# Optimization experiments

Measured on AMD Instinct MI355X. Metric: run time of the kernel, lower is better.

The kernel has to match this reference:

```python
import jax, jax.numpy as jnp
from jax import lax
import numpy as np

B, C, H, W = 16, 128, 128, 128
S1 = C // 2   # 64, LKA3 branch channels
S2 = C - S1   # 64, LKA5 branch channels
EPS = 1e-6
DN = ('NCHW', 'OIHW', 'NCHW')


def _dw(x, w, b, pad, dil=1):
    # depthwise conv; torch weight layout (C,1,kh,kw) == OIHW with groups=C
    y = lax.conv_general_dilated(x, w, (1, 1), [(pad[0], pad[0]), (pad[1], pad[1])],
                                 rhs_dilation=(dil, dil), dimension_numbers=DN,
                                 feature_group_count=w.shape[0])
    return y + b[None, :, None, None]


def _pw(x, w, b):
    # 1x1 pointwise conv
    y = lax.conv_general_dilated(x, w, (1, 1), [(0, 0), (0, 0)], dimension_numbers=DN)
    return y + b[None, :, None, None]


def setup_inputs() -> dict:
    key = jax.random.key(0)
    ks = iter(jax.random.split(key, 40))
    rn = lambda shape, s=0.05: jax.random.normal(next(ks), shape, jnp.float32) * s
    inp = {
        'x': jax.random.normal(next(ks), (B, C, H, W), jnp.float32),
        'ln_w': jnp.ones((C,), jnp.float32),
        'ln_b': jnp.zeros((C,), jnp.float32),
        'scale': rn((1, C, 1, 1)),
        'pf_w': rn((2 * C, C, 1, 1)), 'pf_b': rn((2 * C,)),
        # LKA3: dw(1x3) -> dw(3x1) -> dw5 dil2 -> 1x1
        'lka3_w1': rn((S1, 1, 1, 3)), 'lka3_b1': rn((S1,)),
        'lka3_w2': rn((S1, 1, 3, 1)), 'lka3_b2': rn((S1,)),
        'lka3_w3': rn((S1, 1, 5, 5)), 'lka3_b3': rn((S1,)),
        'lka3_w4': rn((S1, S1, 1, 1)), 'lka3_b4': rn((S1,)),
        # LKA5: dw5 -> dw7 dil2 -> 1x1
        'lka5_w1': rn((S2, 1, 5, 5)), 'lka5_b1': rn((S2,)),
        'lka5_w2': rn((S2, 1, 7, 7)), 'lka5_b2': rn((S2,)),
        'lka5_w3': rn((S2, S2, 1, 1)), 'lka5_b3': rn((S2,)),
        # gating convs
        'x3a_w': rn((S1, 1, 1, 3)), 'x3a_b': rn((S1,)),
        'x3b_w': rn((S1, 1, 3, 1)), 'x3b_b': rn((S1,)),
        'x5_w': rn((S2, 1, 5, 5)), 'x5_b': rn((S2,)),
        'pl_w': rn((C, C, 1, 1)), 'pl_b': rn((C,)),
    }
    return inp


def reference(x, ln_w, ln_b, scale, pf_w, pf_b,
              lka3_w1, lka3_b1, lka3_w2, lka3_b2, lka3_w3, lka3_b3, lka3_w4, lka3_b4,
              lka5_w1, lka5_b1, lka5_w2, lka5_b2, lka5_w3, lka5_b3,
              x3a_w, x3a_b, x3b_w, x3b_b, x5_w, x5_b, pl_w, pl_b):
    shortcut = x
    # channels_first LayerNorm (biased variance over channel dim)
    u = jnp.mean(x, axis=1, keepdims=True)
    s = jnp.mean((x - u) ** 2, axis=1, keepdims=True)
    xn = (x - u) * lax.rsqrt(s + EPS)
    xn = ln_w[None, :, None, None] * xn + ln_b[None, :, None, None]
    # proj_first: C -> 2C
    h = _pw(xn, pf_w, pf_b)
    a, xh = h[:, :C], h[:, C:]
    a1, a2 = a[:, :S1], a[:, S1:]
    # gating branch for a1: 1x3 then 3x1 depthwise
    x3_out = _dw(_dw(a1, x3a_w, x3a_b, (0, 1)), x3b_w, x3b_b, (1, 0))
    # LKA3: dw(1x3)->dw(3x1)->dw5(dil2,pad4)->1x1
    l3 = _dw(a1, lka3_w1, lka3_b1, (0, 1))
    l3 = _dw(l3, lka3_w2, lka3_b2, (1, 0))
    l3 = _dw(l3, lka3_w3, lka3_b3, (4, 4), dil=2)
    l3 = _pw(l3, lka3_w4, lka3_b4)
    attn_1 = l3 * x3_out
    # LKA5: dw5(pad2)->dw7(dil2,pad6)->1x1
    l5 = _dw(a2, lka5_w1, lka5_b1, (2, 2))
    l5 = _dw(l5, lka5_w2, lka5_b2, (6, 6), dil=2)
    l5 = _pw(l5, lka5_w3, lka5_b3)
    attn_2 = l5 * _dw(a2, x5_w, x5_b, (2, 2))
    a = jnp.concatenate([attn_1, attn_2], axis=1)
    out = _pw(xh * a, pl_w, pl_b) * scale + shortcut
    return out
```

## Files before the change

### kernel.cpp

```cpp
#include <hip/hip_runtime.h>
#include <hip/hip_bf16.h>

typedef __hip_bfloat16 bf16;
typedef unsigned short ushort_t;
typedef float f32x4 __attribute__((ext_vector_type(4)));
typedef short bf16x8 __attribute__((ext_vector_type(8)));
typedef ushort_t u16x4 __attribute__((ext_vector_type(4)));

#define MFMA16(a, b, c) __builtin_amdgcn_mfma_f32_16x16x32_bf16(a, b, c, 0, 0, 0)

__device__ inline ushort_t f2b(float f) {
  bf16 h = __float2bfloat16(f);
  return __builtin_bit_cast(ushort_t, h);
}
__device__ inline float b2f(ushort_t u) {
  bf16 h = __builtin_bit_cast(bf16, u);
  return __bfloat162float(h);
}
__device__ inline float blo(unsigned d) { return __builtin_bit_cast(float, d << 16); }
__device__ inline float bhi(unsigned d) { return __builtin_bit_cast(float, d & 0xffff0000u); }


__global__ __launch_bounds__(256) void prepack_pf(
    const float* __restrict__ pf_w, ushort_t* __restrict__ pf_wp)
{
  int idx = blockIdx.x * 256 + threadIdx.x;
  int j = idx & 7, lane = (idx >> 3) & 63, kc = (idx >> 9) & 3, t = idx >> 11;
  int oc = t * 16 + (lane & 15), ic = kc * 32 + (lane >> 4) * 8 + j;
  pf_wp[idx] = f2b(pf_w[oc * 128 + ic]);
}

__global__ __launch_bounds__(256) void prepack_small(
    const float* __restrict__ w4, const float* __restrict__ w5,
    const float* __restrict__ plw, ushort_t* __restrict__ dst)
{
  int idx = blockIdx.x * 256 + threadIdx.x;
  if (idx < 8192) {
    const float* src = (idx < 4096) ? w4 : w5;
    int k = idx & 4095;
    int j = k & 7, lane = (k >> 3) & 63, kc = (k >> 9) & 1, t = k >> 10;
    int oc = t * 16 + (lane & 15), ic = kc * 32 + (lane >> 4) * 8 + j;
    dst[idx] = f2b(src[oc * 64 + ic]);
  } else {
    int k = idx - 8192;
    int j = k & 7, lane = (k >> 3) & 63, kc = (k >> 9) & 3, t = k >> 11;
    int oc = t * 16 + (lane & 15), ic = kc * 32 + (lane >> 4) * 8 + j;
    dst[idx] = f2b(plw[oc * 128 + ic]);
  }
}

__global__ __launch_bounds__(256) void ln_pf_mfma(
    const float* __restrict__ x, const float* __restrict__ ln_w,
    const float* __restrict__ ln_b, const ushort_t* __restrict__ pf_wp,
    const float* __restrict__ pf_b, ushort_t* __restrict__ h)
{
  __shared__ __attribute__((aligned(16))) unsigned char sm[34816];
  ushort_t* xs = (ushort_t*)sm;
  float* red = (float*)(sm + 17408);
  float* mrs = (float*)(sm + 17408 + 2048);

  const int tid = threadIdx.x;
  const int p = tid & 63, cg = tid >> 6;
  const int g0 = blockIdx.x * 64;
  const int b = g0 >> 14, hw0 = g0 & 16383;
  const float* xp = x + (long)b * (128L * 16384) + hw0 + p;

  float v[32];
  #pragma unroll
  for (int i = 0; i < 32; ++i) v[i] = xp[(long)(cg * 32 + i) * 16384];
  float s = 0.f, ss = 0.f;
  #pragma unroll
  for (int i = 0; i < 32; ++i) { s += v[i]; ss += v[i] * v[i]; }
  red[cg * 64 + p] = s;
  red[256 + cg * 64 + p] = ss;
  __syncthreads();
  if (tid < 64) {
    float st = red[tid] + red[64 + tid] + red[128 + tid] + red[192 + tid];
    float sst = red[256 + tid] + red[320 + tid] + red[384 + tid] + red[448 + tid];
    float m = st * 0.0078125f;
    float var = sst * 0.0078125f - m * m;
    mrs[tid] = m;
    mrs[64 + tid] = rsqrtf(var + 1e-6f);
  }
  __syncthreads();
  {
    float m = mrs[p], rs = mrs[64 + p];
    #pragma unroll
    for (int i = 0; i < 32; ++i) {
      int c = cg * 32 + i;
      xs[p * 136 + c] = f2b((v[i] - m) * rs * ln_w[c] + ln_b[c]);
    }
  }
  __syncthreads();

  const int l = tid & 63, lm = l & 15, q = l >> 4;
  const int wv = __builtin_amdgcn_readfirstlane(tid >> 6);
  f32x4 acc[4][4];
  #pragma unroll
  for (int a = 0; a < 4; ++a)
    #pragma unroll
    for (int n = 0; n < 4; ++n) acc[a][n] = {0.f, 0.f, 0.f, 0.f};

  #pragma unroll
  for (int kc = 0; kc < 4; ++kc) {
    bf16x8 af[4], bfr[4];
    #pragma unroll
    for (int mt = 0; mt < 4; ++mt)
      af[mt] = *(const bf16x8*)&xs[(mt * 16 + lm) * 136 + kc * 32 + q * 8];
    #pragma unroll
    for (int nt = 0; nt < 4; ++nt)
      bfr[nt] = *(const bf16x8*)&pf_wp[(((wv * 4 + nt) * 4 + kc) * 64 + l) * 8];
    #pragma unroll
    for (int mt = 0; mt < 4; ++mt)
      #pragma unroll
      for (int nt = 0; nt < 4; ++nt)
        acc[mt][nt] = MFMA16(af[mt], bfr[nt], acc[mt][nt]);
  }
  __syncthreads();

  ushort_t* hst = (ushort_t*)sm;
  #pragma unroll
  for (int nt = 0; nt < 4; ++nt) {
    int oc = wv * 64 + nt * 16 + lm;
    float bias = pf_b[oc];
    #pragma unroll
    for (int mt = 0; mt < 4; ++mt) {
      int px0 = mt * 16 + q * 4;
      union { ushort_t u[4]; uint2 w; } pk;
      #pragma unroll
      for (int r = 0; r < 4; ++r) pk.u[r] = f2b(acc[mt][nt][r] + bias);
      *(uint2*)&hst[oc * 68 + px0] = pk.w;
    }
  }
  __syncthreads();
  {
    int px = (tid & 31) * 2;
    int ocb = tid >> 5;
    ushort_t* hp = h + (long)b * 256 * 16384 + hw0 + px;
    #pragma unroll
    for (int i = 0; i < 32; ++i) {
      int oc = ocb + 8 * i;
      *(unsigned*)(hp + (long)oc * 16384) = *(unsigned*)&hst[oc * 68 + px];
    }
  }
}

__global__ __launch_bounds__(256) void dw_branch1_kernel(
    const bf16* __restrict__ hbuf,
    const float* __restrict__ w1, const float* __restrict__ b1,
    const float* __restrict__ w2, const float* __restrict__ b2,
    const float* __restrict__ w3, const float* __restrict__ b3,
    const float* __restrict__ wa, const float* __restrict__ ba,
    const float* __restrict__ wb, const float* __restrict__ bb,
    bf16* __restrict__ d3, bf16* __restrict__ x3o)
{
  __shared__ __attribute__((aligned(16))) unsigned char smem[28000];
  float* st1 = (float*)smem;
  float* st2 = (float*)(smem + 14560);
  ushort_t* sa = (ushort_t*)(smem + 14560);
  unsigned* sad = (unsigned*)sa;

  const int t = blockIdx.x;
  const int band = t & 7, c = (t >> 3) & 63, b = t >> 9;
  const int y0 = band * 16;
  const int tid = threadIdx.x;
  const bf16* ap = hbuf + ((long)b * 256 + c) * 16384;

  for (int i = tid; i < 26 * 16; i += 256) {
    int r = i >> 4, j = i & 15;
    int dw = (j < 4) ? j : (64 + j);
    sad[r * 80 + dw] = 0u;
  }
  {
    const int lane = tid & 63, w = tid >> 6;
    #pragma unroll
    for (int i = 0; i < 7; ++i) {
      int rr = w + 4 * i;
      if (rr < 26) {
        int gy = y0 - 5 + rr;
        unsigned val = 0u;
        if ((unsigned)gy < 128u) val = *(const unsigned*)(ap + gy * 128 + lane * 2);
        sad[rr * 80 + 4 + lane] = val;
      }
    }
  }
  __syncthreads();

  {
    float W0 = w1[c * 3], Wm = w1[c * 3 + 1], Wp = w1[c * 3 + 2];
    const float B1v = b1[c];
    for (int task = tid; task < 26 * 17; task += 256) {
      int r = task / 17, g = task - r * 17;
      int c0 = g * 8;
      const unsigned* sr = sad + r * 80 + (c0 >> 1) + 1;
      unsigned e0 = sr[0], e1 = sr[1], e2 = sr[2], e3 = sr[3], e4 = sr[4], e5 = sr[5];
      float vw[12];
      vw[0] = blo(e0); vw[1] = bhi(e0); vw[2] = blo(e1); vw[3] = bhi(e1);
      vw[4] = blo(e2); vw[5] = bhi(e2); vw[6] = blo(e3); vw[7] = bhi(e3);
      vw[8] = blo(e4); vw[9] = bhi(e4); vw[10] = blo(e5); vw[11] = bhi(e5);
      int gy = y0 - 5 + r;
      bool rok = (unsigned)gy < 128u;
      float* dst = &st1[r * 140 + c0];
      #pragma unroll
      for (int j = 0; j < 8; ++j) {
        float v = W0 * vw[j + 1] + Wm * vw[j + 2] + Wp * vw[j + 3] + B1v;
        int xx = c0 - 4 + j;
        dst[j] = (rok && (unsigned)xx < 128u) ? v : 0.f;
      }
    }
  }

  const int tx = tid & 15, ty = tid >> 4;
  const int x0 = tx * 8;
  const int y = y0 + ty;

  {
    float A0 = wa[c * 3], A1 = wa[c * 3 + 1], A2 = wa[c * 3 + 2];
    float Bv0 = wb[c * 3], Bv1 = wb[c * 3 + 1], Bv2 = wb[c * 3 + 2];
    const float BAv = ba[c], BBv = bb[c];
    float su[3][8];
    #pragma unroll
    for (int dy = 0; dy < 3; ++dy) {
      int gy2 = y - 1 + dy;
      int srow = ty + 4 + dy;
      const unsigned* sr = sad + srow * 80 + (x0 >> 1) + 3;
      unsigned e0 = sr[0], e1 = sr[1], e2 = sr[2], e3 = sr[3], e4 = sr[4], e5 = sr[5];
      float vw[12];
      vw[0] = blo(e0); vw[1] = bhi(e0); vw[2] = blo(e1); vw[3] = bhi(e1);
      vw[4] = blo(e2); vw[5] = bhi(e2); vw[6] = blo(e3); vw[7] = bhi(e3);
      vw[8] = blo(e4); vw[9] = bhi(e4); vw[10] = blo(e5); vw[11] = bhi(e5);
      bool rok = (unsigned)gy2 < 128u;
      #pragma unroll
      for (int j = 0; j < 8; ++j) {
        float v = A0 * vw[j + 1] + A1 * vw[j + 2] + A2 * vw[j + 3] + BAv;
        su[dy][j] = rok ? v : 0.f;
      }
    }
    union { ushort_t u[8]; uint4 v; } pk;
    #pragma unroll
    for (int j = 0; j < 8; ++j)
      pk.u[j] = f2b(Bv0 * su[0][j] + Bv1 * su[1][j] + Bv2 * su[2][j] + BBv);
    bf16* x3p = x3o + ((long)b * 64 + c) * 16384;
    *(uint4*)(x3p + y * 128 + x0) = pk.v;
  }
  __syncthreads();

  {
    float W0 = w2[c * 3], Wm = w2[c * 3 + 1], Wp = w2[c * 3 + 2];
    const float B2v = b2[c];
    for (int task = tid; task < 24 * 17; task += 256) {
      int q = task / 17, g = task - q * 17;
      int c0 = g * 8;
      const float* r0 = &st1[q * 140 + c0];
      const float* r1 = &st1[(q + 1) * 140 + c0];
      const float* r2 = &st1[(q + 2) * 140 + c0];
      int gy = y0 - 4 + q;
      bool rok = (unsigned)gy < 128u;
      float* dst = &st2[q * 140 + c0];
      #pragma unroll
      for (int j = 0; j < 8; ++j) {
        float v = W0 * r0[j] + Wm * r1[j] + Wp * r2[j] + B2v;
        int xx = c0 - 4 + j;
        dst[j] = (rok && (unsigned)xx < 128u) ? v : 0.f;
      }
    }
  }
  __syncthreads();

  {
    float W[25];
    #pragma unroll
    for (int k = 0; k < 25; ++k) W[k] = w3[c * 25 + k];
    float acc[8];
    #pragma unroll
    for (int j = 0; j < 8; ++j) acc[j] = b3[c];
    #pragma unroll
    for (int u = 0; u < 5; ++u) {
      const float* svr = &st2[(ty + 2 * u) * 140 + x0];
      float vw[16];
      #pragma unroll
      for (int k = 0; k < 16; ++k) vw[k] = svr[k];
      #pragma unroll
      for (int vv = 0; vv < 5; ++vv)
        #pragma unroll
        for (int j = 0; j < 8; ++j)
          acc[j] += W[u * 5 + vv] * vw[j + 2 * vv];
    }
    union { ushort_t u[8]; uint4 v; } pk;
    #pragma unroll
    for (int j = 0; j < 8; ++j) pk.u[j] = f2b(acc[j]);
    bf16* d3p = d3 + ((long)b * 64 + c) * 16384;
    *(uint4*)(d3p + y * 128 + x0) = pk.v;
  }
}

__global__ __launch_bounds__(256) void dw_branch2_kernel(
    const bf16* __restrict__ hbuf,
    const float* __restrict__ w1, const float* __restrict__ b1,
    const float* __restrict__ w2, const float* __restrict__ b2,
    const float* __restrict__ w5, const float* __restrict__ b5,
    bf16* __restrict__ d5, bf16* __restrict__ x5o)
{
  __shared__ ushort_t sa[32 * 160];
  __shared__ float sv[28 * 148];

  const int t = blockIdx.x;
  const int band = t & 7, c = (t >> 3) & 63, b = t >> 9;
  const int y0 = band * 16;
  const int tid = threadIdx.x;
  const bf16* ap = hbuf + ((long)b * 256 + 64 + c) * 16384;

  unsigned* sad = (unsigned*)sa;
  for (int i = tid; i < 32 * 16; i += 256) {
    int r = i >> 4, j = i & 15;
    int dw = (j < 4) ? j : (64 + j);
    sad[r * 80 + dw] = 0u;
  }
  {
    const int lane = tid & 63, w = tid >> 6;
    #pragma unroll
    for (int i = 0; i < 8; ++i) {
      int rr = w + 4 * i;
      int gy = y0 - 8 + rr;
      unsigned val = 0u;
      if ((unsigned)gy < 128u) val = *(const unsigned*)(ap + gy * 128 + lane * 2);
      sad[rr * 80 + 4 + lane] = val;
    }
  }
  __syncthreads();

  {
    float W[25];
    #pragma unroll
    for (int k = 0; k < 25; ++k) W[k] = w1[c * 25 + k];
    const float B1v = b1[c];
    for (int task = tid; task < 28 * 18; task += 256) {
      int r = task / 18, g = task - r * 18;
      int c0 = g * 8;
      float acc[8];
      #pragma unroll
      for (int j = 0; j < 8; ++j) acc[j] = B1v;
      #pragma unroll
      for (int u = 0; u < 5; ++u) {
        const unsigned* sr = sad + (r + u) * 80 + (c0 >> 1);
        unsigned e0 = sr[0], e1 = sr[1], e2 = sr[2], e3 = sr[3], e4 = sr[4], e5 = sr[5];
        float vw[12];
        vw[0] = blo(e0); vw[1] = bhi(e0); vw[2] = blo(e1); vw[3] = bhi(e1);
        vw[4] = blo(e2); vw[5] = bhi(e2); vw[6] = blo(e3); vw[7] = bhi(e3);
        vw[8] = blo(e4); vw[9] = bhi(e4); vw[10] = blo(e5); vw[11] = bhi(e5);
        #pragma unroll
        for (int v5 = 0; v5 < 5; ++v5)
          #pragma unroll
          for (int j = 0; j < 8; ++j)
            acc[j] += W[u * 5 + v5] * vw[j + v5];
      }
      int gy = y0 - 6 + r;
      bool rok = (unsigned)gy < 128u;
      float* svr = &sv[r * 148 + c0];
      #pragma unroll
      for (int j = 0; j < 8; ++j) {
        int xx = c0 + j - 6;
        svr[j] = (rok && (unsigned)xx < 128u) ? acc[j] : 0.f;
      }
    }
  }

  const int tx = tid & 15, ty = tid >> 4;
  const int x0 = tx * 8;
  const int y = y0 + ty;

  {
    float W[25];
    #pragma unroll
    for (int k = 0; k < 25; ++k) W[k] = w5[c * 25 + k];
    float acc[8];
    #pragma unroll
    for (int j = 0; j < 8; ++j) acc[j] = b5[c];
    #pragma unroll
    for (int u = 0; u < 5; ++u) {
      const unsigned* sr = sad + (ty + 6 + u) * 80 + (x0 >> 1);
      unsigned e0 = sr[3], e1 = sr[4], e2 = sr[5], e3 = sr[6], e4 = sr[7], e5 = sr[8];
      float vw[12];
      vw[0] = blo(e0); vw[1] = bhi(e0); vw[2] = blo(e1); vw[3] = bhi(e1);
      vw[4] = blo(e2); vw[5] = bhi(e2); vw[6] = blo(e3); vw[7] = bhi(e3);
      vw[8] = blo(e4); vw[9] = bhi(e4); vw[10] = blo(e5); vw[11] = bhi(e5);
      #pragma unroll
      for (int v5 = 0; v5 < 5; ++v5)
        #pragma unroll
        for (int j = 0; j < 8; ++j)
          acc[j] += W[u * 5 + v5] * vw[j + v5];
    }
    union { ushort_t u[8]; uint4 v; } pk;
    #pragma unroll
    for (int j = 0; j < 8; ++j) pk.u[j] = f2b(acc[j]);
    bf16* x5p = x5o + ((long)b * 64 + c) * 16384;
    *(uint4*)(x5p + y * 128 + x0) = pk.v;
  }
  __syncthreads();

  {
    float W[49];
    #pragma unroll
    for (int k = 0; k < 49; ++k) W[k] = w2[c * 49 + k];
    float acc[8];
    #pragma unroll
    for (int j = 0; j < 8; ++j) acc[j] = b2[c];
    #pragma unroll
    for (int u = 0; u < 7; ++u) {
      const float* svr = &sv[(ty + 2 * u) * 148 + x0];
      float vw[20];
      #pragma unroll
      for (int k = 0; k < 20; ++k) vw[k] = svr[k];
      #pragma unroll
      for (int vv = 0; vv < 7; ++vv)
        #pragma unroll
        for (int j = 0; j < 8; ++j)
          acc[j] += W[u * 7 + vv] * vw[j + 2 * vv];
    }
    union { ushort_t u[8]; uint4 v; } pk;
    #pragma unroll
    for (int j = 0; j < 8; ++j) pk.u[j] = f2b(acc[j]);
    bf16* d5p = d5 + ((long)b * 64 + c) * 16384;
    *(uint4*)(d5p + y * 128 + x0) = pk.v;
  }
}

__global__ __launch_bounds__(256) void final_mfma(
    const ushort_t* __restrict__ h, const ushort_t* __restrict__ d3,
    const ushort_t* __restrict__ x3o, const ushort_t* __restrict__ d5,
    const ushort_t* __restrict__ x5o,
    const ushort_t* __restrict__ w4p, const float* __restrict__ b4,
    const ushort_t* __restrict__ w5p, const float* __restrict__ b5,
    const ushort_t* __restrict__ plwp, const float* __restrict__ plb,
    const float* __restrict__ scale, const float* __restrict__ x,
    float* __restrict__ out)
{
  __shared__ __attribute__((aligned(16))) unsigned char sm[53248];
  ushort_t* A3 = (ushort_t*)sm;
  ushort_t* A5 = (ushort_t*)(sm + 9216);
  ushort_t* gA = (ushort_t*)sm;
  ushort_t* X3 = (ushort_t*)(sm + 18432);
  ushort_t* X5 = (ushort_t*)(sm + 27136);
  ushort_t* XH = (ushort_t*)(sm + 35840);
  float* outL  = (float*)(sm + 18432);

  const int tid = threadIdx.x;
  const int g0 = blockIdx.x * 64;
  const int b = g0 >> 14, hw0 = g0 & 16383;
  const long base64 = (long)b * 64 * 16384 + hw0;
  const long base256 = (long)b * 256 * 16384 + hw0;
  const int p = tid & 63;
  const int p2 = (tid & 31) * 2, cg8 = tid >> 5;

  unsigned xhreg[16];
  #pragma unroll
  for (int i = 0; i < 16; ++i) {
    int ch = cg8 + 8 * i;
    xhreg[i] = *(const unsigned*)&h[base256 + (long)(128 + ch) * 16384 + p2];
  }

  #pragma unroll
  for (int i = 0; i < 8; ++i) {
    int ch = (tid >> 6) * 2 + 8 * i;
    unsigned v3 = (unsigned)d3[base64 + (long)ch * 16384 + p] |
                  ((unsigned)d3[base64 + (long)(ch + 1) * 16384 + p] << 16);
    unsigned v5 = (unsigned)d5[base64 + (long)ch * 16384 + p] |
                  ((unsigned)d5[base64 + (long)(ch + 1) * 16384 + p] << 16);
    *(unsigned*)&A3[p * 72 + ch] = v3;
    *(unsigned*)&A5[p * 72 + ch] = v5;
  }
  #pragma unroll
  for (int i = 0; i < 8; ++i) {
    int ch = cg8 + 8 * i;
    *(unsigned*)&X3[ch * 68 + p2] = *(const unsigned*)&x3o[base64 + (long)ch * 16384 + p2];
    *(unsigned*)&X5[ch * 68 + p2] = *(const unsigned*)&x5o[base64 + (long)ch * 16384 + p2];
  }
  __syncthreads();

  const int l = tid & 63, lm = l & 15, q = l >> 4;
  const int wv = __builtin_amdgcn_readfirstlane(tid >> 6);

  f32x4 ac1[4], ac2[4];
  #pragma unroll
  for (int n = 0; n < 4; ++n) { ac1[n] = {0.f,0.f,0.f,0.f}; ac2[n] = {0.f,0.f,0.f,0.f}; }
  #pragma unroll
  for (int kc = 0; kc < 2; ++kc) {
    bf16x8 a3f = *(const bf16x8*)&A3[(wv * 16 + lm) * 72 + kc * 32 + q * 8];
    bf16x8 a5f = *(const bf16x8*)&A5[(wv * 16 + lm) * 72 + kc * 32 + q * 8];
    #pragma unroll
    for (int nt = 0; nt < 4; ++nt) {
      bf16x8 bw4 = *(const bf16x8*)&w4p[((nt * 2 + kc) * 64 + l) * 8];
      bf16x8 bw5 = *(const bf16x8*)&w5p[((nt * 2 + kc) * 64 + l) * 8];
      ac1[nt] = MFMA16(a3f, bw4, ac1[nt]);
      ac2[nt] = MFMA16(a5f, bw5, ac2[nt]);
    }
  }

  #pragma unroll
  for (int i = 0; i < 16; ++i) {
    int ch = cg8 + 8 * i;
    *(unsigned*)&XH[ch * 68 + p2] = xhreg[i];
  }
  __syncthreads();

  {
    const int pxb = wv * 16 + q * 4;
    #pragma unroll
    for (int nt = 0; nt < 4; ++nt) {
      int oc = nt * 16 + lm;
      float bb1 = b4[oc], bb2 = b5[oc];
      u16x4 x3v = *(const u16x4*)&X3[oc * 68 + pxb];
      u16x4 x5v = *(const u16x4*)&X5[oc * 68 + pxb];
      u16x4 h1v = *(const u16x4*)&XH[oc * 68 + pxb];
      u16x4 h2v = *(const u16x4*)&XH[(64 + oc) * 68 + pxb];
      #pragma unroll
      for (int r = 0; r < 4; ++r) {
        float at1 = (ac1[nt][r] + bb1) * b2f(x3v[r]);
        float at2 = (ac2[nt][r] + bb2) * b2f(x5v[r]);
        float g1 = b2f(h1v[r]) * at1;
        float g2 = b2f(h2v[r]) * at2;
        gA[(pxb + r) * 136 + oc]      = f2b(g1);
        gA[(pxb + r) * 136 + 64 + oc] = f2b(g2);
      }
    }
  }
  __syncthreads();

  f32x4 ap[4][2];
  #pragma unroll
  for (int mt = 0; mt < 4; ++mt) { ap[mt][0] = {0.f,0.f,0.f,0.f}; ap[mt][1] = {0.f,0.f,0.f,0.f}; }
  #pragma unroll
  for (int kc = 0; kc < 4; ++kc) {
    bf16x8 af[4];
    #pragma unroll
    for (int mt = 0; mt < 4; ++mt)
      af[mt] = *(const bf16x8*)&gA[(mt * 16 + lm) * 136 + kc * 32 + q * 8];
    #pragma unroll
    for (int j = 0; j < 2; ++j) {
      bf16x8 bp = *(const bf16x8*)&plwp[(((wv * 2 + j) * 4 + kc) * 64 + l) * 8];
      #pragma unroll
      for (int mt = 0; mt < 4; ++mt)
        ap[mt][j] = MFMA16(af[mt], bp, ap[mt][j]);
    }
  }
  #pragma unroll
  for (int j = 0; j < 2; ++j) {
    int oc = (wv * 2 + j) * 16 + lm;
    float sc = scale[oc], bb = plb[oc];
    #pragma unroll
    for (int mt = 0; mt < 4; ++mt) {
      int px0 = mt * 16 + q * 4;
      f32x4 vv;
      #pragma unroll
      for (int r = 0; r < 4; ++r) vv[r] = (ap[mt][j][r] + bb) * sc;
      *(f32x4*)&outL[oc * 68 + px0] = vv;
    }
  }
  __syncthreads();
  {
    const float* xp = x + (long)b * 128 * 16384 + hw0 + p;
    float* op = out + (long)b * 128 * 16384 + hw0 + p;
    #pragma unroll
    for (int i = 0; i < 32; ++i) {
      int oc = (tid >> 6) + 4 * i;
      op[(long)oc * 16384] = outL[oc * 68 + p] + xp[(long)oc * 16384];
    }
  }
}

extern "C" void kernel_launch(void* const* d_in, const int* in_sizes, int n_in,
                              void* d_out, int out_size, void* d_ws, size_t ws_size,
                              hipStream_t stream)
{
  (void)in_sizes; (void)n_in; (void)out_size; (void)ws_size;
  const float* x       = (const float*)d_in[0];
  const float* ln_w    = (const float*)d_in[1];
  const float* ln_b    = (const float*)d_in[2];
  const float* scale   = (const float*)d_in[3];
  const float* pf_w    = (const float*)d_in[4];
  const float* pf_b    = (const float*)d_in[5];
  const float* lka3_w1 = (const float*)d_in[6];
  const float* lka3_b1 = (const float*)d_in[7];
  const float* lka3_w2 = (const float*)d_in[8];
  const float* lka3_b2 = (const float*)d_in[9];
  const float* lka3_w3 = (const float*)d_in[10];
  const float* lka3_b3 = (const float*)d_in[11];
  const float* lka3_w4 = (const float*)d_in[12];
  const float* lka3_b4 = (const float*)d_in[13];
  const float* lka5_w1 = (const float*)d_in[14];
  const float* lka5_b1 = (const float*)d_in[15];
  const float* lka5_w2 = (const float*)d_in[16];
  const float* lka5_b2 = (const float*)d_in[17];
  const float* lka5_w3 = (const float*)d_in[18];
  const float* lka5_b3 = (const float*)d_in[19];
  const float* x3a_w   = (const float*)d_in[20];
  const float* x3a_b   = (const float*)d_in[21];
  const float* x3b_w   = (const float*)d_in[22];
  const float* x3b_b   = (const float*)d_in[23];
  const float* x5_w    = (const float*)d_in[24];
  const float* x5_b    = (const float*)d_in[25];
  const float* pl_w    = (const float*)d_in[26];
  const float* pl_b    = (const float*)d_in[27];
  float* out = (float*)d_out;

  bf16* h   = (bf16*)d_ws;
  bf16* d3  = h + 67108864L;
  bf16* x3o = d3 + 16777216L;
  bf16* d5  = x3o + 16777216L;
  bf16* x5o = d5 + 16777216L;
  ushort_t* pf_wp = (ushort_t*)d_out;
  ushort_t* wsmall = (ushort_t*)d_ws;

  dim3 blk(256);

  prepack_pf<<<128, blk, 0, stream>>>(pf_w, pf_wp);
  ln_pf_mfma<<<4096, blk, 0, stream>>>(x, ln_w, ln_b, pf_wp, pf_b, (ushort_t*)h);

  dw_branch1_kernel<<<8192, blk, 0, stream>>>(
      h, lka3_w1, lka3_b1, lka3_w2, lka3_b2, lka3_w3, lka3_b3,
      x3a_w, x3a_b, x3b_w, x3b_b, d3, x3o);

  dw_branch2_kernel<<<8192, blk, 0, stream>>>(
      h, lka5_w1, lka5_b1, lka5_w2, lka5_b2, x5_w, x5_b, d5, x5o);

  prepack_small<<<96, blk, 0, stream>>>(lka3_w4, lka5_w3, pl_w, wsmall);

  final_mfma<<<4096, blk, 0, stream>>>(
      (const ushort_t*)h, (const ushort_t*)d3, (const ushort_t*)x3o,
      (const ushort_t*)d5, (const ushort_t*)x5o,
      wsmall, lka3_b4, wsmall + 4096, lka5_b3,
      wsmall + 8192, pl_b, scale, x, out);
}
```

Measured before the change: 519.5 us.

## Merge depthwise branch kernels into one launch and read xh directly from global

```diff
diff --git a/kernel.cpp b/kernel.cpp
--- a/kernel.cpp
+++ b/kernel.cpp
@@ -145,283 +145,281 @@
   }
 }
 
-__global__ __launch_bounds__(256) void dw_branch1_kernel(
+__global__ __launch_bounds__(256) void dw_both_kernel(
     const bf16* __restrict__ hbuf,
-    const float* __restrict__ w1, const float* __restrict__ b1,
-    const float* __restrict__ w2, const float* __restrict__ b2,
-    const float* __restrict__ w3, const float* __restrict__ b3,
+    const float* __restrict__ w1a, const float* __restrict__ b1a,
+    const float* __restrict__ w2a, const float* __restrict__ b2a,
+    const float* __restrict__ w3a, const float* __restrict__ b3a,
     const float* __restrict__ wa, const float* __restrict__ ba,
     const float* __restrict__ wb, const float* __restrict__ bb,
-    bf16* __restrict__ d3, bf16* __restrict__ x3o)
+    bf16* __restrict__ d3, bf16* __restrict__ x3o,
+    const float* __restrict__ w1b, const float* __restrict__ b1b,
+    const float* __restrict__ w2b, const float* __restrict__ b2b,
+    const float* __restrict__ w5b, const float* __restrict__ b5b,
+    bf16* __restrict__ d5, bf16* __restrict__ x5o)
 {
   __shared__ __attribute__((aligned(16))) unsigned char smem[28000];
-  float* st1 = (float*)smem;
-  float* st2 = (float*)(smem + 14560);
-  ushort_t* sa = (ushort_t*)(smem + 14560);
-  unsigned* sad = (unsigned*)sa;
-
-  const int t = blockIdx.x;
-  const int band = t & 7, c = (t >> 3) & 63, b = t >> 9;
-  const int y0 = band * 16;
   const int tid = threadIdx.x;
-  const bf16* ap = hbuf + ((long)b * 256 + c) * 16384;
-
-  for (int i = tid; i < 26 * 16; i += 256) {
-    int r = i >> 4, j = i & 15;
-    int dw = (j < 4) ? j : (64 + j);
-    sad[r * 80 + dw] = 0u;
-  }
-  {
-    const int lane = tid & 63, w = tid >> 6;
-    #pragma unroll
-    for (int i = 0; i < 7; ++i) {
-      int rr = w + 4 * i;
-      if (rr < 26) {
-        int gy = y0 - 5 + rr;
-        unsigned val = 0u;
-        if ((unsigned)gy < 128u) val = *(const unsigned*)(ap + gy * 128 + lane * 2);
-        sad[rr * 80 + 4 + lane] = val;
-      }
-    }
-  }
-  __syncthreads();
-
-  {
-    float W0 = w1[c * 3], Wm = w1[c * 3 + 1], Wp = w1[c * 3 + 2];
-    const float B1v = b1[c];
-    for (int task = tid; task < 26 * 17; task += 256) {
-      int r = task / 17, g = task - r * 17;
-      int c0 = g * 8;
-      const unsigned* sr = sad + r * 80 + (c0 >> 1) + 1;
-      unsigned e0 = sr[0], e1 = sr[1], e2 = sr[2], e3 = sr[3], e4 = sr[4], e5 = sr[5];
-      float vw[12];
-      vw[0] = blo(e0); vw[1] = bhi(e0); vw[2] = blo(e1); vw[3] = bhi(e1);
-      vw[4] = blo(e2); vw[5] = bhi(e2); vw[6] = blo(e3); vw[7] = bhi(e3);
-      vw[8] = blo(e4); vw[9] = bhi(e4); vw[10] = blo(e5); vw[11] = bhi(e5);
-      int gy = y0 - 5 + r;
-      bool rok = (unsigned)gy < 128u;
-      float* dst = &st1[r * 140 + c0];
-      #pragma unroll
-      for (int j = 0; j < 8; ++j) {
-        float v = W0 * vw[j + 1] + Wm * vw[j + 2] + Wp * vw[j + 3] + B1v;
-        int xx = c0 - 4 + j;
-        dst[j] = (rok && (unsigned)xx < 128u) ? v : 0.f;
-      }
-    }
-  }
-
-  const int tx = tid & 15, ty = tid >> 4;
-  const int x0 = tx * 8;
-  const int y = y0 + ty;
-
-  {
-    float A0 = wa[c * 3], A1 = wa[c * 3 + 1], A2 = wa[c * 3 + 2];
-    float Bv0 = wb[c * 3], Bv1 = wb[c * 3 + 1], Bv2 = wb[c * 3 + 2];
-    const float BAv = ba[c], BBv = bb[c];
-    float su[3][8];
-    #pragma unroll
-    for (int dy = 0; dy < 3; ++dy) {
-      int gy2 = y - 1 + dy;
-      int srow = ty + 4 + dy;
-      const unsigned* sr = sad + srow * 80 + (x0 >> 1) + 3;
-      unsigned e0 = sr[0], e1 = sr[1], e2 = sr[2], e3 = sr[3], e4 = sr[4], e5 = sr[5];
-      float vw[12];
-      vw[0] = blo(e0); vw[1] = bhi(e0); vw[2] = blo(e1); vw[3] = bhi(e1);
-      vw[4] = blo(e2); vw[5] = bhi(e2); vw[6] = blo(e3); vw[7] = bhi(e3);
-      vw[8] = blo(e4); vw[9] = bhi(e4); vw[10] = blo(e5); vw[11] = bhi(e5);
-      bool rok = (unsigned)gy2 < 128u;
-      #pragma unroll
-      for (int j = 0; j < 8; ++j) {
-        float v = A0 * vw[j + 1] + A1 * vw[j + 2] + A2 * vw[j + 3] + BAv;
-        su[dy][j] = rok ? v : 0.f;
-      }
-    }
-    union { ushort_t u[8]; uint4 v; } pk;
-    #pragma unroll
-    for (int j = 0; j < 8; ++j)
-      pk.u[j] = f2b(Bv0 * su[0][j] + Bv1 * su[1][j] + Bv2 * su[2][j] + BBv);
-    bf16* x3p = x3o + ((long)b * 64 + c) * 16384;
-    *(uint4*)(x3p + y * 128 + x0) = pk.v;
-  }
-  __syncthreads();
-
-  {
-    float W0 = w2[c * 3], Wm = w2[c * 3 + 1], Wp = w2[c * 3 + 2];
-    const float B2v = b2[c];
-    for (int task = tid; task < 24 * 17; task += 256) {
-      int q = task / 17, g = task - q * 17;
-      int c0 = g * 8;
-      const float* r0 = &st1[q * 140 + c0];
-      const float* r1 = &st1[(q + 1) * 140 + c0];
-      const float* r2 = &st1[(q + 2) * 140 + c0];
-      int gy = y0 - 4 + q;
-      bool rok = (unsigned)gy < 128u;
-      float* dst = &st2[q * 140 + c0];
-      #pragma unroll
-      for (int j = 0; j < 8; ++j) {
-        float v = W0 * r0[j] + Wm * r1[j] + Wp * r2[j] + B2v;
-        int xx = c0 - 4 + j;
-        dst[j] = (rok && (unsigned)xx < 128u) ? v : 0.f;
-      }
-    }
-  }
-  __syncthreads();
-
-  {
-    float W[25];
-    #pragma unroll
-    for (int k = 0; k < 25; ++k) W[k] = w3[c * 25 + k];
-    float acc[8];
-    #pragma unroll
-    for (int j = 0; j < 8; ++j) acc[j] = b3[c];
-    #pragma unroll
-    for (int u = 0; u < 5; ++u) {
-      const float* svr = &st2[(ty + 2 * u) * 140 + x0];
-      float vw[16];
-      #pragma unroll
-      for (int k = 0; k < 16; ++k) vw[k] = svr[k];
-      #pragma unroll
-      for (int vv = 0; vv < 5; ++vv)
-        #pragma unroll
-        for (int j = 0; j < 8; ++j)
-          acc[j] += W[u * 5 + vv] * vw[j + 2 * vv];
-    }
-    union { ushort_t u[8]; uint4 v; } pk;
-    #pragma unroll
-    for (int j = 0; j < 8; ++j) pk.u[j] = f2b(acc[j]);
-    bf16* d3p = d3 + ((long)b * 64 + c) * 16384;
-    *(uint4*)(d3p + y * 128 + x0) = pk.v;
-  }
-}
-
-__global__ __launch_bounds__(256) void dw_branch2_kernel(
-    const bf16* __restrict__ hbuf,
-    const float* __restrict__ w1, const float* __restrict__ b1,
-    const float* __restrict__ w2, const float* __restrict__ b2,
-    const float* __restrict__ w5, const float* __restrict__ b5,
-    bf16* __restrict__ d5, bf16* __restrict__ x5o)
-{
-  __shared__ ushort_t sa[32 * 160];
-  __shared__ float sv[28 * 148];
-
-  const int t = blockIdx.x;
-  const int band = t & 7, c = (t >> 3) & 63, b = t >> 9;
-  const int y0 = band * 16;
-  const int tid = threadIdx.x;
-  const bf16* ap = hbuf + ((long)b * 256 + 64 + c) * 16384;
-
-  unsigned* sad = (unsigned*)sa;
-  for (int i = tid; i < 32 * 16; i += 256) {
-    int r = i >> 4, j = i & 15;
-    int dw = (j < 4) ? j : (64 + j);
-    sad[r * 80 + dw] = 0u;
-  }
-  {
-    const int lane = tid & 63, w = tid >> 6;
-    #pragma unroll
-    for (int i = 0; i < 8; ++i) {
-      int rr = w + 4 * i;
-      int gy = y0 - 8 + rr;
-      unsigned val = 0u;
-      if ((unsigned)gy < 128u) val = *(const unsigned*)(ap + gy * 128 + lane * 2);
-      sad[rr * 80 + 4 + lane] = val;
-    }
-  }
-  __syncthreads();
-
-  {
-    float W[25];
-    #pragma unroll
-    for (int k = 0; k < 25; ++k) W[k] = w1[c * 25 + k];
-    const float B1v = b1[c];
-    for (int task = tid; task < 28 * 18; task += 256) {
-      int r = task / 18, g = task - r * 18;
-      int c0 = g * 8;
-      float acc[8];
-      #pragma unroll
-      for (int j = 0; j < 8; ++j) acc[j] = B1v;
-      #pragma unroll
-      for (int u = 0; u < 5; ++u) {
-        const unsigned* sr = sad + (r + u) * 80 + (c0 >> 1);
+
+  if (blockIdx.x < 8192) {
+    float* st1 = (float*)smem;
+    float* st2 = (float*)(smem + 14560);
+    ushort_t* sa = (ushort_t*)(smem + 14560);
+    unsigned* sad = (unsigned*)sa;
+
+    const int t = blockIdx.x;
+    const int band = t & 7, c = (t >> 3) & 63, b = t >> 9;
+    const int y0 = band * 16;
+    const bf16* ap = hbuf + ((long)b * 256 + c) * 16384;
+
+    for (int i = tid; i < 26 * 16; i += 256) {
+      int r = i >> 4, j = i & 15;
+      int dw = (j < 4) ? j : (64 + j);
+      sad[r * 80 + dw] = 0u;
+    }
+    {
+      const int lane = tid & 63, w = tid >> 6;
+      #pragma unroll
+      for (int i = 0; i < 7; ++i) {
+        int rr = w + 4 * i;
+        if (rr < 26) {
+          int gy = y0 - 5 + rr;
+          unsigned val = 0u;
+          if ((unsigned)gy < 128u) val = *(const unsigned*)(ap + gy * 128 + lane * 2);
+          sad[rr * 80 + 4 + lane] = val;
+        }
+      }
+    }
+    __syncthreads();
+
+    {
+      float W0 = w1a[c * 3], Wm = w1a[c * 3 + 1], Wp = w1a[c * 3 + 2];
+      const float B1v = b1a[c];
+      for (int task = tid; task < 26 * 17; task += 256) {
+        int r = task / 17, g = task - r * 17;
+        int c0 = g * 8;
+        const unsigned* sr = sad + r * 80 + (c0 >> 1) + 1;
         unsigned e0 = sr[0], e1 = sr[1], e2 = sr[2], e3 = sr[3], e4 = sr[4], e5 = sr[5];
         float vw[12];
         vw[0] = blo(e0); vw[1] = bhi(e0); vw[2] = blo(e1); vw[3] = bhi(e1);
         vw[4] = blo(e2); vw[5] = bhi(e2); vw[6] = blo(e3); vw[7] = bhi(e3);
         vw[8] = blo(e4); vw[9] = bhi(e4); vw[10] = blo(e5); vw[11] = bhi(e5);
+        int gy = y0 - 5 + r;
+        bool rok = (unsigned)gy < 128u;
+        float* dst = &st1[r * 140 + c0];
+        #pragma unroll
+        for (int j = 0; j < 8; ++j) {
+          float v = W0 * vw[j + 1] + Wm * vw[j + 2] + Wp * vw[j + 3] + B1v;
+          int xx = c0 - 4 + j;
+          dst[j] = (rok && (unsigned)xx < 128u) ? v : 0.f;
+        }
+      }
+    }
+
+    const int tx = tid & 15, ty = tid >> 4;
+    const int x0 = tx * 8;
+    const int y = y0 + ty;
+
+    {
+      float A0 = wa[c * 3], A1 = wa[c * 3 + 1], A2 = wa[c * 3 + 2];
+      float Bv0 = wb[c * 3], Bv1 = wb[c * 3 + 1], Bv2 = wb[c * 3 + 2];
+      const float BAv = ba[c], BBv = bb[c];
+      float su[3][8];
+      #pragma unroll
+      for (int dy = 0; dy < 3; ++dy) {
+        int gy2 = y - 1 + dy;
+        int srow = ty + 4 + dy;
+        const unsigned* sr = sad + srow * 80 + (x0 >> 1) + 3;
+        unsigned e0 = sr[0], e1 = sr[1], e2 = sr[2], e3 = sr[3], e4 = sr[4], e5 = sr[5];
+        float vw[12];
+        vw[0] = blo(e0); vw[1] = bhi(e0); vw[2] = blo(e1); vw[3] = bhi(e1);
+        vw[4] = blo(e2); vw[5] = bhi(e2); vw[6] = blo(e3); vw[7] = bhi(e3);
+        vw[8] = blo(e4); vw[9] = bhi(e4); vw[10] = blo(e5); vw[11] = bhi(e5);
+        bool rok = (unsigned)gy2 < 128u;
+        #pragma unroll
+        for (int j = 0; j < 8; ++j) {
+          float v = A0 * vw[j + 1] + A1 * vw[j + 2] + A2 * vw[j + 3] + BAv;
+          su[dy][j] = rok ? v : 0.f;
+        }
+      }
+      union { ushort_t u[8]; uint4 v; } pk;
+      #pragma unroll
+      for (int j = 0; j < 8; ++j)
+        pk.u[j] = f2b(Bv0 * su[0][j] + Bv1 * su[1][j] + Bv2 * su[2][j] + BBv);
+      bf16* x3p = x3o + ((long)b * 64 + c) * 16384;
+      *(uint4*)(x3p + y * 128 + x0) = pk.v;
+    }
+    __syncthreads();
+
+    {
+      float W0 = w2a[c * 3], Wm = w2a[c * 3 + 1], Wp = w2a[c * 3 + 2];
+      const float B2v = b2a[c];
+      for (int task = tid; task < 24 * 17; task += 256) {
+        int q = task / 17, g = task - q * 17;
+        int c0 = g * 8;
+        const float* r0 = &st1[q * 140 + c0];
+        const float* r1 = &st1[(q + 1) * 140 + c0];
+        const float* r2 = &st1[(q + 2) * 140 + c0];
+        int gy = y0 - 4 + q;
+        bool rok = (unsigned)gy < 128u;
+        float* dst = &st2[q * 140 + c0];
+        #pragma unroll
+        for (int j = 0; j < 8; ++j) {
+          float v = W0 * r0[j] + Wm * r1[j] + Wp * r2[j] + B2v;
+          int xx = c0 - 4 + j;
+          dst[j] = (rok && (unsigned)xx < 128u) ? v : 0.f;
+        }
+      }
+    }
+    __syncthreads();
+
+    {
+      float W[25];
+      #pragma unroll
+      for (int k = 0; k < 25; ++k) W[k] = w3a[c * 25 + k];
+      float acc[8];
+      #pragma unroll
+      for (int j = 0; j < 8; ++j) acc[j] = b3a[c];
+      #pragma unroll
+      for (int u = 0; u < 5; ++u) {
+        const float* svr = &st2[(ty + 2 * u) * 140 + x0];
+        float vw[16];
+        #pragma unroll
+        for (int k = 0; k < 16; ++k) vw[k] = svr[k];
+        #pragma unroll
+        for (int vv = 0; vv < 5; ++vv)
+          #pragma unroll
+          for (int j = 0; j < 8; ++j)
+            acc[j] += W[u * 5 + vv] * vw[j + 2 * vv];
+      }
+      union { ushort_t u[8]; uint4 v; } pk;
+      #pragma unroll
+      for (int j = 0; j < 8; ++j) pk.u[j] = f2b(acc[j]);
+      bf16* d3p = d3 + ((long)b * 64 + c) * 16384;
+      *(uint4*)(d3p + y * 128 + x0) = pk.v;
+    }
+  } else {
+    ushort_t* sa = (ushort_t*)smem;
+    float* sv = (float*)(smem + 10240);
+    unsigned* sad = (unsigned*)sa;
+
+    const int t = blockIdx.x - 8192;
+    const int band = t & 7, c = (t >> 3) & 63, b = t >> 9;
+    const int y0 = band * 16;
+    const bf16* ap = hbuf + ((long)b * 256 + 64 + c) * 16384;
+
+    for (int i = tid; i < 32 * 16; i += 256) {
+      int r = i >> 4, j = i & 15;
+      int dw = (j < 4) ? j : (64 + j);
+      sad[r * 80 + dw] = 0u;
+    }
+    {
+      const int lane = tid & 63, w = tid >> 6;
+      #pragma unroll
+      for (int i = 0; i < 8; ++i) {
+        int rr = w + 4 * i;
+        int gy = y0 - 8 + rr;
+        unsigned val = 0u;
+        if ((unsigned)gy < 128u) val = *(const unsigned*)(ap + gy * 128 + lane * 2);
+        sad[rr * 80 + 4 + lane] = val;
+      }
+    }
+    __syncthreads();
+
+    {
+      float W[25];
+      #pragma unroll
+      for (int k = 0; k < 25; ++k) W[k] = w1b[c * 25 + k];
+      const float B1v = b1b[c];
+      for (int task = tid; task < 28 * 18; task += 256) {
+        int r = task / 18, g = task - r * 18;
+        int c0 = g * 8;
+        float acc[8];
+        #pragma unroll
+        for (int j = 0; j < 8; ++j) acc[j] = B1v;
+        #pragma unroll
+        for (int u = 0; u < 5; ++u) {
+          const unsigned* sr = sad + (r + u) * 80 + (c0 >> 1);
+          unsigned e0 = sr[0], e1 = sr[1], e2 = sr[2], e3 = sr[3], e4 = sr[4], e5 = sr[5];
+          float vw[12];
+          vw[0] = blo(e0); vw[1] = bhi(e0); vw[2] = blo(e1); vw[3] = bhi(e1);
+          vw[4] = blo(e2); vw[5] = bhi(e2); vw[6] = blo(e3); vw[7] = bhi(e3);
+          vw[8] = blo(e4); vw[9] = bhi(e4); vw[10] = blo(e5); vw[11] = bhi(e5);
+          #pragma unroll
+          for (int v5 = 0; v5 < 5; ++v5)
+            #pragma unroll
+            for (int j = 0; j < 8; ++j)
+              acc[j] += W[u * 5 + v5] * vw[j + v5];
+        }
+        int gy = y0 - 6 + r;
+        bool rok = (unsigned)gy < 128u;
+        float* svr = &sv[r * 148 + c0];
+        #pragma unroll
+        for (int j = 0; j < 8; ++j) {
+          int xx = c0 + j - 6;
+          svr[j] = (rok && (unsigned)xx < 128u) ? acc[j] : 0.f;
+        }
+      }
+    }
+
+    const int tx = tid & 15, ty = tid >> 4;
+    const int x0 = tx * 8;
+    const int y = y0 + ty;
+
+    {
+      float W[25];
+      #pragma unroll
+      for (int k = 0; k < 25; ++k) W[k] = w5b[c * 25 + k];
+      float acc[8];
+      #pragma unroll
+      for (int j = 0; j < 8; ++j) acc[j] = b5b[c];
+      #pragma unroll
+      for (int u = 0; u < 5; ++u) {
+        const unsigned* sr = sad + (ty + 6 + u) * 80 + (x0 >> 1);
+        unsigned e0 = sr[3], e1 = sr[4], e2 = sr[5], e3 = sr[6], e4 = sr[7], e5 = sr[8];
+        float vw[12];
+        vw[0] = blo(e0); vw[1] = bhi(e0); vw[2] = blo(e1); vw[3] = bhi(e1);
+        vw[4] = blo(e2); vw[5] = bhi(e2); vw[6] = blo(e3); vw[7] = bhi(e3);
+        vw[8] = blo(e4); vw[9] = bhi(e4); vw[10] = blo(e5); vw[11] = bhi(e5);
         #pragma unroll
         for (int v5 = 0; v5 < 5; ++v5)
           #pragma unroll
           for (int j = 0; j < 8; ++j)
             acc[j] += W[u * 5 + v5] * vw[j + v5];
       }
-      int gy = y0 - 6 + r;
-      bool rok = (unsigned)gy < 128u;
-      float* svr = &sv[r * 148 + c0];
-      #pragma unroll
-      for (int j = 0; j < 8; ++j) {
-        int xx = c0 + j - 6;
-        svr[j] = (rok && (unsigned)xx < 128u) ? acc[j] : 0.f;
-      }
-    }
-  }
-
-  const int tx = tid & 15, ty = tid >> 4;
-  const int x0 = tx * 8;
-  const int y = y0 + ty;
-
-  {
-    float W[25];
-    #pragma unroll
-    for (int k = 0; k < 25; ++k) W[k] = w5[c * 25 + k];
-    float acc[8];
-    #pragma unroll
-    for (int j = 0; j < 8; ++j) acc[j] = b5[c];
-    #pragma unroll
-    for (int u = 0; u < 5; ++u) {
-      const unsigned* sr = sad + (ty + 6 + u) * 80 + (x0 >> 1);
-      unsigned e0 = sr[3], e1 = sr[4], e2 = sr[5], e3 = sr[6], e4 = sr[7], e5 = sr[8];
-      float vw[12];
-      vw[0] = blo(e0); vw[1] = bhi(e0); vw[2] = blo(e1); vw[3] = bhi(e1);
-      vw[4] = blo(e2); vw[5] = bhi(e2); vw[6] = blo(e3); vw[7] = bhi(e3);
-      vw[8] = blo(e4); vw[9] = bhi(e4); vw[10] = blo(e5); vw[11] = bhi(e5);
-      #pragma unroll
-      for (int v5 = 0; v5 < 5; ++v5)
-        #pragma unroll
-        for (int j = 0; j < 8; ++j)
-          acc[j] += W[u * 5 + v5] * vw[j + v5];
-    }
-    union { ushort_t u[8]; uint4 v; } pk;
-    #pragma unroll
-    for (int j = 0; j < 8; ++j) pk.u[j] = f2b(acc[j]);
-    bf16* x5p = x5o + ((long)b * 64 + c) * 16384;
-    *(uint4*)(x5p + y * 128 + x0) = pk.v;
-  }
-  __syncthreads();
-
-  {
-    float W[49];
-    #pragma unroll
-    for (int k = 0; k < 49; ++k) W[k] = w2[c * 49 + k];
-    float acc[8];
-    #pragma unroll
-    for (int j = 0; j < 8; ++j) acc[j] = b2[c];
-    #pragma unroll
-    for (int u = 0; u < 7; ++u) {
-      const float* svr = &sv[(ty + 2 * u) * 148 + x0];
-      float vw[20];
-      #pragma unroll
-      for (int k = 0; k < 20; ++k) vw[k] = svr[k];
-      #pragma unroll
-      for (int vv = 0; vv < 7; ++vv)
-        #pragma unroll
-        for (int j = 0; j < 8; ++j)
-          acc[j] += W[u * 7 + vv] * vw[j + 2 * vv];
-    }
-    union { ushort_t u[8]; uint4 v; } pk;
-    #pragma unroll
-    for (int j = 0; j < 8; ++j) pk.u[j] = f2b(acc[j]);
-    bf16* d5p = d5 + ((long)b * 64 + c) * 16384;
-    *(uint4*)(d5p + y * 128 + x0) = pk.v;
+      union { ushort_t u[8]; uint4 v; } pk;
+      #pragma unroll
+      for (int j = 0; j < 8; ++j) pk.u[j] = f2b(acc[j]);
+      bf16* x5p = x5o + ((long)b * 64 + c) * 16384;
+      *(uint4*)(x5p + y * 128 + x0) = pk.v;
+    }
+    __syncthreads();
+
+    {
+      float W[49];
+      #pragma unroll
+      for (int k = 0; k < 49; ++k) W[k] = w2b[c * 49 + k];
+      float acc[8];
+      #pragma unroll
+      for (int j = 0; j < 8; ++j) acc[j] = b2b[c];
+      #pragma unroll
+      for (int u = 0; u < 7; ++u) {
+        const float* svr = &sv[(ty + 2 * u) * 148 + x0];
+        float vw[20];
+        #pragma unroll
+        for (int k = 0; k < 20; ++k) vw[k] = svr[k];
+        #pragma unroll
+        for (int vv = 0; vv < 7; ++vv)
+          #pragma unroll
+          for (int j = 0; j < 8; ++j)
+            acc[j] += W[u * 7 + vv] * vw[j + 2 * vv];
+      }
+      union { ushort_t u[8]; uint4 v; } pk;
+      #pragma unroll
+      for (int j = 0; j < 8; ++j) pk.u[j] = f2b(acc[j]);
+      bf16* d5p = d5 + ((long)b * 64 + c) * 16384;
+      *(uint4*)(d5p + y * 128 + x0) = pk.v;
+    }
   }
 }
 
@@ -435,14 +433,13 @@
     const float* __restrict__ scale, const float* __restrict__ x,
     float* __restrict__ out)
 {
-  __shared__ __attribute__((aligned(16))) unsigned char sm[53248];
+  __shared__ __attribute__((aligned(16))) unsigned char sm[35840];
   ushort_t* A3 = (ushort_t*)sm;
   ushort_t* A5 = (ushort_t*)(sm + 9216);
   ushort_t* gA = (ushort_t*)sm;
   ushort_t* X3 = (ushort_t*)(sm + 18432);
   ushort_t* X5 = (ushort_t*)(sm + 27136);
-  ushort_t* XH = (ushort_t*)(sm + 35840);
-  float* outL  = (float*)(sm + 18432);
+  float* outL  = (float*)sm;
 
   const int tid = threadIdx.x;
   const int g0 = blockIdx.x * 64;
@@ -451,13 +448,6 @@
   const long base256 = (long)b * 256 * 16384 + hw0;
   const int p = tid & 63;
   const int p2 = (tid & 31) * 2, cg8 = tid >> 5;
-
-  unsigned xhreg[16];
-  #pragma unroll
-  for (int i = 0; i < 16; ++i) {
-    int ch = cg8 + 8 * i;
-    xhreg[i] = *(const unsigned*)&h[base256 + (long)(128 + ch) * 16384 + p2];
-  }
 
   #pragma unroll
   for (int i = 0; i < 8; ++i) {
@@ -495,12 +485,6 @@
       ac2[nt] = MFMA16(a5f, bw5, ac2[nt]);
     }
   }
-
-  #pragma unroll
-  for (int i = 0; i < 16; ++i) {
-    int ch = cg8 + 8 * i;
-    *(unsigned*)&XH[ch * 68 + p2] = xhreg[i];
-  }
   __syncthreads();
 
   {
@@ -511,8 +495,8 @@
       float bb1 = b4[oc], bb2 = b5[oc];
       u16x4 x3v = *(const u16x4*)&X3[oc * 68 + pxb];
       u16x4 x5v = *(const u16x4*)&X5[oc * 68 + pxb];
-      u16x4 h1v = *(const u16x4*)&XH[oc * 68 + pxb];
-      u16x4 h2v = *(const u16x4*)&XH[(64 + oc) * 68 + pxb];
+      u16x4 h1v = *(const u16x4*)&h[base256 + (long)(128 + oc) * 16384 + pxb];
+      u16x4 h2v = *(const u16x4*)&h[base256 + (long)(192 + oc) * 16384 + pxb];
       #pragma unroll
       for (int r = 0; r < 4; ++r) {
         float at1 = (ac1[nt][r] + bb1) * b2f(x3v[r]);
@@ -543,6 +527,8 @@
         ap[mt][j] = MFMA16(af[mt], bp, ap[mt][j]);
     }
   }
+  __syncthreads();
+
   #pragma unroll
   for (int j = 0; j < 2; ++j) {
     int oc = (wv * 2 + j) * 16 + lm;
@@ -616,12 +602,10 @@
   prepack_pf<<<128, blk, 0, stream>>>(pf_w, pf_wp);
   ln_pf_mfma<<<4096, blk, 0, stream>>>(x, ln_w, ln_b, pf_wp, pf_b, (ushort_t*)h);
 
-  dw_branch1_kernel<<<8192, blk, 0, stream>>>(
+  dw_both_kernel<<<16384, blk, 0, stream>>>(
       h, lka3_w1, lka3_b1, lka3_w2, lka3_b2, lka3_w3, lka3_b3,
-      x3a_w, x3a_b, x3b_w, x3b_b, d3, x3o);
-
-  dw_branch2_kernel<<<8192, blk, 0, stream>>>(
-      h, lka5_w1, lka5_b1, lka5_w2, lka5_b2, x5_w, x5_b, d5, x5o);
+      x3a_w, x3a_b, x3b_w, x3b_b, d3, x3o,
+      lka5_w1, lka5_b1, lka5_w2, lka5_b2, x5_w, x5_b, d5, x5o);
 
   prepack_small<<<96, blk, 0, stream>>>(lka3_w4, lka5_w3, pl_w, wsmall);
 
```

After: 569.3 us. +9.6%, slower.
